# Optimization experiments

Hardware: AMD Instinct MI355X
Metric: run time of the kernel (lower is better)

The kernel has to match this reference:

```python
import jax, jax.numpy as jnp
from jax import lax
import numpy as np

B, H, W, C = 64, 224, 224, 3
OH, OW = 224, 224
EPS = 1e-3  # keras BatchNormalization default epsilon
FLAT = 52 * 52 * 10  # after conv7(valid)->pool2->conv5(valid)->pool2 on 224x224


def setup_inputs() -> dict:
    key = jax.random.key(0)
    ks = jax.random.split(key, 6)
    return {
        "x": jax.random.normal(ks[0], (B, H, W, C), jnp.float32),
        "c1_w": jax.random.normal(ks[1], (7, 7, C, 8), jnp.float32) * 0.05,
        "c1_b": jnp.zeros((8,), jnp.float32),
        "g1": jnp.ones((8,), jnp.float32),
        "b1": jnp.zeros((8,), jnp.float32),
        "m1": jnp.zeros((8,), jnp.float32),
        "v1": jnp.ones((8,), jnp.float32),
        "c2_w": jax.random.normal(ks[2], (5, 5, 8, 10), jnp.float32) * 0.05,
        "c2_b": jnp.zeros((10,), jnp.float32),
        "g2": jnp.ones((10,), jnp.float32),
        "b2": jnp.zeros((10,), jnp.float32),
        "m2": jnp.zeros((10,), jnp.float32),
        "v2": jnp.ones((10,), jnp.float32),
        "d1_w": jax.random.normal(ks[3], (FLAT, 32), jnp.float32) * 0.01,
        "d1_b": jnp.zeros((32,), jnp.float32),
        "d2_w": jax.random.normal(ks[4], (32, 6), jnp.float32) * 0.01,
        "d2_b": jnp.array([1.0, 0.0, 0.0, 0.0, 1.0, 0.0], jnp.float32),  # identity affine
    }


def _conv(x, w, b):
    return lax.conv_general_dilated(x, w, (1, 1), 'VALID',
                                    dimension_numbers=('NHWC', 'HWIO', 'NHWC')) + b


def _maxpool(x):
    return lax.reduce_window(x, -jnp.inf, lax.max, (1, 2, 2, 1), (1, 2, 2, 1), 'VALID')


def _bn(x, g, b, m, v):
    # inference-mode batchnorm: gamma*(x-mean)/sqrt(var+eps)+beta
    return (x - m) * lax.rsqrt(v + EPS) * g + b


def _bilinear(img, px, py):
    # img: [H,W,C]; px,py: [OH,OW] pixel-space sample coords; zero fill outside
    x0 = jnp.floor(px).astype(jnp.int32)
    y0 = jnp.floor(py).astype(jnp.int32)

    def gather(yi, xi):
        valid = (yi >= 0) & (yi < H) & (xi >= 0) & (xi < W)
        v = img[jnp.clip(yi, 0, H - 1), jnp.clip(xi, 0, W - 1)]  # [OH,OW,C]
        return v * valid[..., None]

    wx = (px - x0)[..., None]
    wy = (py - y0)[..., None]
    return (gather(y0, x0) * (1 - wx) * (1 - wy)
            + gather(y0, x0 + 1) * wx * (1 - wy)
            + gather(y0 + 1, x0) * (1 - wx) * wy
            + gather(y0 + 1, x0 + 1) * wx * wy)


def reference(x, c1_w, c1_b, g1, b1, m1, v1, c2_w, c2_b, g2, b2, m2, v2,
              d1_w, d1_b, d2_w, d2_b):
    # localization network
    h = _maxpool(_bn(jax.nn.relu(_conv(x, c1_w, c1_b)), g1, b1, m1, v1))
    h = _maxpool(_bn(jax.nn.relu(_conv(h, c2_w, c2_b)), g2, b2, m2, v2))
    h = h.reshape(h.shape[0], -1)                      # [B, FLAT]
    h = jax.nn.relu(h @ d1_w + d1_b)                   # [B, 32]
    theta = (h @ d2_w + d2_b).reshape(-1, 2, 3)        # [B, 2, 3]

    # normalized homogeneous grid [N,3] with N = OH*OW
    xs = jnp.linspace(-1.0, 1.0, OW)
    ys = jnp.linspace(-1.0, 1.0, OH)
    xg, yg = jnp.meshgrid(xs, ys)
    grid = jnp.stack([xg.ravel(), yg.ravel(), jnp.ones(OH * OW, jnp.float32)], axis=-1)

    coords = jnp.einsum('bij,nj->bni', theta, grid)    # [B, N, 2]
    px = ((coords[..., 0] + 1.0) * 0.5 * (W - 1)).reshape(-1, OH, OW)
    py = ((coords[..., 1] + 1.0) * 0.5 * (H - 1)).reshape(-1, OH, OW)
    return jax.vmap(_bilinear)(x, px, py)              # [B, OH, OW, C]
```

## Files before the change

kernel.cpp:

```cpp
#include <hip/hip_runtime.h>
#include <hip/hip_bf16.h>


#define NCHUNK 423
#define KC 64

__global__ __launch_bounds__(256, 8) void k_conv1(
    const float* __restrict__ x, const float* __restrict__ w,
    const float* __restrict__ bias, const float* __restrict__ g,
    const float* __restrict__ bt, const float* __restrict__ m,
    const float* __restrict__ v, float* __restrict__ out, int zbase) {
  __shared__ float s_in[3][38][42];
  __shared__ float s_bn[3][8];
  const int tid = threadIdx.x;
  const int bx = blockIdx.x, by = blockIdx.y, b = zbase + blockIdx.z;

  if (tid < 8) {
    float sc = g[tid] * rsqrtf(v[tid] + 1e-3f);
    s_bn[0][tid] = sc;
    s_bn[1][tid] = bt[tid] - m[tid] * sc;
    s_bn[2][tid] = bias[tid];
  }
  const int iy0 = by * 32, ix0 = bx * 32;
  const float* xb = x + (size_t)b * 224 * 224 * 3;
  for (int f = tid; f < 38 * 114; f += 256) {
    int r = f / 114, rem = f - r * 114;
    int q = rem / 3, c = rem - q * 3;
    int gy = iy0 + r; if (gy > 223) gy = 223;
    int gc = ix0 + q; if (gc > 223) gc = 223;
    s_in[c][r][q] = xb[(gy * 224 + gc) * 3 + c];
  }
  __syncthreads();

  const int pxl = tid & 15, pyl = tid >> 4;
  const int lx = 2 * pxl, ly = 2 * pyl;
  float acc[2][2][8];
#pragma unroll
  for (int pr = 0; pr < 2; ++pr)
#pragma unroll
    for (int pc = 0; pc < 2; ++pc)
#pragma unroll
      for (int co = 0; co < 8; ++co) acc[pr][pc][co] = 0.f;

#pragma unroll 1
  for (int ci = 0; ci < 3; ++ci) {
    float rw[8][8];
#pragma unroll
    for (int r = 0; r < 8; ++r)
#pragma unroll
      for (int j = 0; j < 4; ++j) {
        float2 t = *(const float2*)&s_in[ci][ly + r][lx + 2 * j];
        rw[r][2 * j] = t.x; rw[r][2 * j + 1] = t.y;
      }
#pragma unroll
    for (int ky = 0; ky < 7; ++ky) {
      float wv[7][8];
#pragma unroll
      for (int kx = 0; kx < 7; ++kx) {
        const float* wp = w + ((ky * 7 + kx) * 3 + ci) * 8;
        float4 a = *(const float4*)wp;
        float4 c4 = *(const float4*)(wp + 4);
        wv[kx][0] = a.x;  wv[kx][1] = a.y;  wv[kx][2] = a.z;  wv[kx][3] = a.w;
        wv[kx][4] = c4.x; wv[kx][5] = c4.y; wv[kx][6] = c4.z; wv[kx][7] = c4.w;
      }
#pragma unroll
      for (int kx = 0; kx < 7; ++kx)
#pragma unroll
        for (int pr = 0; pr < 2; ++pr)
#pragma unroll
          for (int pc = 0; pc < 2; ++pc) {
            float iv = rw[ky + pr][kx + pc];
#pragma unroll
            for (int co = 0; co < 8; ++co)
              acc[pr][pc][co] = fmaf(iv, wv[kx][co], acc[pr][pc][co]);
          }
    }
  }

  const int py = by * 16 + pyl, px = bx * 16 + pxl;
  if (py < 109 && px < 109) {
#pragma unroll
    for (int co = 0; co < 8; ++co) {
      float sc = s_bn[0][co], sh = s_bn[1][co], bs = s_bn[2][co];
      float a0 = fmaxf(acc[0][0][co] + bs, 0.f) * sc + sh;
      float a1 = fmaxf(acc[0][1][co] + bs, 0.f) * sc + sh;
      float a2 = fmaxf(acc[1][0][co] + bs, 0.f) * sc + sh;
      float a3 = fmaxf(acc[1][1][co] + bs, 0.f) * sc + sh;
      out[((size_t)co * 64 + b) * 109 * 110 + py * 110 + px] =
          fmaxf(fmaxf(a0, a1), fmaxf(a2, a3));
    }
  }
}

__global__ __launch_bounds__(256) void k_conv2(
    const float* __restrict__ in, const float* __restrict__ w,
    const float* __restrict__ bias, const float* __restrict__ g,
    const float* __restrict__ bt, const float* __restrict__ m,
    const float* __restrict__ v, float* __restrict__ out) {
  __shared__ float s_in[8][36][38];
  __shared__ float s_bn[3][10];
  const int tid = threadIdx.x;
  const int bx = blockIdx.x, by = blockIdx.y, b = blockIdx.z;

  if (tid < 10) {
    float sc = g[tid] * rsqrtf(v[tid] + 1e-3f);
    s_bn[0][tid] = sc;
    s_bn[1][tid] = bt[tid] - m[tid] * sc;
    s_bn[2][tid] = bias[tid];
  }
  const int iy0 = by * 32, ix0 = bx * 32;
  for (int f = tid; f < 8 * 36 * 36; f += 256) {
    int ci = f / 1296, rem = f - ci * 1296;
    int r = rem / 36, q = rem - r * 36;
    int gy = iy0 + r; if (gy > 108) gy = 108;
    int gc = ix0 + q; if (gc > 108) gc = 108;
    s_in[ci][r][q] = in[(((size_t)ci * 64 + b) * 109 + gy) * 110 + gc];
  }
  __syncthreads();

  const int pxl = tid & 15, pyl = tid >> 4;
  const int lx = 2 * pxl, ly = 2 * pyl;
  float acc[2][2][10];
#pragma unroll
  for (int pr = 0; pr < 2; ++pr)
#pragma unroll
    for (int pc = 0; pc < 2; ++pc)
#pragma unroll
      for (int co = 0; co < 10; ++co) acc[pr][pc][co] = 0.f;

#pragma unroll 1
  for (int ci = 0; ci < 8; ++ci) {
    float rw[6][8];
#pragma unroll
    for (int r = 0; r < 6; ++r)
#pragma unroll
      for (int j = 0; j < 4; ++j) {
        float2 t = *(const float2*)&s_in[ci][ly + r][lx + 2 * j];
        rw[r][2 * j] = t.x; rw[r][2 * j + 1] = t.y;
      }
#pragma unroll
    for (int ky = 0; ky < 5; ++ky) {
      float wv[5][10];
#pragma unroll
      for (int kx = 0; kx < 5; ++kx) {
        const float* wp = w + ((ky * 5 + kx) * 8 + ci) * 10;
#pragma unroll
        for (int u = 0; u < 5; ++u) {
          float2 t = *(const float2*)(wp + 2 * u);
          wv[kx][2 * u] = t.x; wv[kx][2 * u + 1] = t.y;
        }
      }
#pragma unroll
      for (int kx = 0; kx < 5; ++kx)
#pragma unroll
        for (int pr = 0; pr < 2; ++pr)
#pragma unroll
          for (int pc = 0; pc < 2; ++pc) {
            float iv = rw[ky + pr][kx + pc];
#pragma unroll
            for (int co = 0; co < 10; ++co)
              acc[pr][pc][co] = fmaf(iv, wv[kx][co], acc[pr][pc][co]);
          }
    }
  }

  const int py = by * 16 + pyl, px = bx * 16 + pxl;
  if (py < 52 && px < 52) {
    float res[10];
#pragma unroll
    for (int co = 0; co < 10; ++co) {
      float sc = s_bn[0][co], sh = s_bn[1][co], bs = s_bn[2][co];
      float a0 = fmaxf(acc[0][0][co] + bs, 0.f) * sc + sh;
      float a1 = fmaxf(acc[0][1][co] + bs, 0.f) * sc + sh;
      float a2 = fmaxf(acc[1][0][co] + bs, 0.f) * sc + sh;
      float a3 = fmaxf(acc[1][1][co] + bs, 0.f) * sc + sh;
      res[co] = fmaxf(fmaxf(a0, a1), fmaxf(a2, a3));
    }
    float2* op2 = (float2*)&out[(((size_t)b * 52 + py) * 52 + px) * 10];
#pragma unroll
    for (int i = 0; i < 5; i++)
      op2[i] = make_float2(res[2 * i], res[2 * i + 1]);
  }
}

__global__ __launch_bounds__(256) void k_fc1(
    const float* __restrict__ act, const float* __restrict__ w,
    float* __restrict__ partial) {
  __shared__ float s_a[64][KC];
  __shared__ float s_w[KC * 32];
  const int tid = threadIdx.x;
  const int chunk = blockIdx.x;
  const int k0 = chunk * KC;
  for (int f = tid; f < 64 * KC; f += 256) {
    int row = f >> 6, j = f & (KC - 1);
    int k = k0 + j;
    s_a[row][j] = (k < 27040) ? act[(size_t)row * 27040 + k] : 0.f;
  }
  for (int f = tid; f < KC * 32; f += 256) {
    int k = k0 + (f >> 5);
    s_w[f] = (k < 27040) ? w[(size_t)k0 * 32 + f] : 0.f;
  }
  __syncthreads();
  const int o = tid & 31, gg = tid >> 5;
  float sums[8];
#pragma unroll
  for (int i = 0; i < 8; i++) sums[i] = 0.f;
#pragma unroll 2
  for (int j = 0; j < KC; j += 4) {
    float w0 = s_w[j * 32 + o];
    float w1 = s_w[(j + 1) * 32 + o];
    float w2 = s_w[(j + 2) * 32 + o];
    float w3 = s_w[(j + 3) * 32 + o];
#pragma unroll
    for (int i = 0; i < 8; i++) {
      float4 av = *(const float4*)&s_a[gg * 8 + i][j];
      sums[i] = fmaf(av.x, w0, sums[i]);
      sums[i] = fmaf(av.y, w1, sums[i]);
      sums[i] = fmaf(av.z, w2, sums[i]);
      sums[i] = fmaf(av.w, w3, sums[i]);
    }
  }
#pragma unroll
  for (int i = 0; i < 8; i++)
    partial[((size_t)chunk * 64 + gg * 8 + i) * 32 + o] = sums[i];
}

__global__ __launch_bounds__(256) void k_fc2(
    const float* __restrict__ partial, const float* __restrict__ d1b,
    const float* __restrict__ d2w, const float* __restrict__ d2b,
    float* __restrict__ theta) {
  const int b = blockIdx.x;
  const int t = threadIdx.x;
  const int o = t & 31, seg = t >> 5;
  const int c0 = (seg < 7) ? seg * 53 : 371;
  const int cnt = (seg < 7) ? 53 : 52;
  float s = 0.f;
  for (int c = c0; c < c0 + cnt; ++c)
    s += partial[((size_t)c * 64 + b) * 32 + o];
  __shared__ float s_red[8][33];
  s_red[seg][o] = s;
  __syncthreads();
  __shared__ float s_h[32];
  if (t < 32) {
    float tot = 0.f;
#pragma unroll
    for (int sg = 0; sg < 8; ++sg) tot += s_red[sg][t];
    s_h[t] = fmaxf(tot + d1b[t], 0.f);
  }
  __syncthreads();
  if (t < 6) {
    float th = d2b[t];
#pragma unroll
    for (int o2 = 0; o2 < 32; o2++) th = fmaf(s_h[o2], d2w[o2 * 6 + t], th);
    theta[b * 6 + t] = th;
  }
}

__global__ __launch_bounds__(256) void k_sample(
    const float* __restrict__ x, const float* __restrict__ theta,
    float* __restrict__ out) {
  const int b = blockIdx.y;
  __shared__ float th[6];
  if (threadIdx.x < 6) th[threadIdx.x] = theta[b * 6 + threadIdx.x];
  __syncthreads();
  const int t = blockIdx.x * 256 + threadIdx.x;
  const int oy = t / 224, ox = t - oy * 224;
  const float xn = -1.f + (2.f / 223.f) * (float)ox;
  const float yn = -1.f + (2.f / 223.f) * (float)oy;
  const float cx = th[0] * xn + th[1] * yn + th[2];
  const float cy = th[3] * xn + th[4] * yn + th[5];
  const float px = (cx + 1.f) * 0.5f * 223.f;
  const float py = (cy + 1.f) * 0.5f * 223.f;
  const float x0f = floorf(px), y0f = floorf(py);
  const int x0 = (int)x0f, y0 = (int)y0f;
  const float wx = px - x0f, wy = py - y0f;
  const float* xb = x + (size_t)b * 224 * 224 * 3;
  float a0 = 0.f, a1 = 0.f, a2 = 0.f;
#pragma unroll
  for (int dy = 0; dy < 2; dy++) {
    const int yi = y0 + dy;
    const bool vy = (yi >= 0) && (yi < 224);
    const int yc = yi < 0 ? 0 : (yi > 223 ? 223 : yi);
    const float wyv = dy ? wy : 1.f - wy;
#pragma unroll
    for (int dx = 0; dx < 2; dx++) {
      const int xi = x0 + dx;
      const bool vx = (xi >= 0) && (xi < 224);
      const int xc = xi < 0 ? 0 : (xi > 223 ? 223 : xi);
      const float wv = wyv * (dx ? wx : 1.f - wx) * ((vx && vy) ? 1.f : 0.f);
      const float* p = &xb[(yc * 224 + xc) * 3];
      a0 = fmaf(p[0], wv, a0);
      a1 = fmaf(p[1], wv, a1);
      a2 = fmaf(p[2], wv, a2);
    }
  }
  float* op = &out[((size_t)b * 50176 + t) * 3];
  op[0] = a0; op[1] = a1; op[2] = a2;
}

extern "C" void kernel_launch(void* const* d_in, const int* in_sizes, int n_in,
                              void* d_out, int out_size, void* d_ws, size_t ws_size,
                              hipStream_t stream) {
  const float* x    = (const float*)d_in[0];
  const float* c1w  = (const float*)d_in[1];
  const float* c1b  = (const float*)d_in[2];
  const float* g1   = (const float*)d_in[3];
  const float* b1   = (const float*)d_in[4];
  const float* m1   = (const float*)d_in[5];
  const float* v1   = (const float*)d_in[6];
  const float* c2w  = (const float*)d_in[7];
  const float* c2b  = (const float*)d_in[8];
  const float* g2   = (const float*)d_in[9];
  const float* b2   = (const float*)d_in[10];
  const float* m2   = (const float*)d_in[11];
  const float* v2   = (const float*)d_in[12];
  const float* d1w  = (const float*)d_in[13];
  const float* d1b  = (const float*)d_in[14];
  const float* d2w  = (const float*)d_in[15];
  const float* d2b  = (const float*)d_in[16];
  float* out = (float*)d_out;

  float* ws = (float*)d_ws;
  float* p1    = ws;
  float* p2    = p1 + 6138880;
  float* theta = p2 + 1730560;
  float* part  = ws;

  for (int zb = 0; zb < 64; zb += 16)
    k_conv1<<<dim3(7, 7, 16), 256, 0, stream>>>(x, c1w, c1b, g1, b1, m1, v1, p1, zb);
  k_conv2<<<dim3(4, 4, 64), 256, 0, stream>>>(p1, c2w, c2b, g2, b2, m2, v2, p2);
  k_fc1<<<NCHUNK, 256, 0, stream>>>(p2, d1w, part);
  k_fc2<<<64, 256, 0, stream>>>(part, d1b, d2w, d2b, theta);
  k_sample<<<dim3(196, 64), 256, 0, stream>>>(x, theta, out);
}
```

Measured before the change: 328.3 us.

## Merge conv1 launches, retile conv2 by full-width row strips, vectorize sampler stores

conv1 now runs as a single launch over all 64 images instead of four launches, and its occupancy hint is dropped. conv2 is retiled into full-width 8-row strips that load the input channels in two halves of four. This removes the wasted halo and padding of the old 4x4 tile grid, but leaves 12 of every 64 threads idle. The sampler computes two output pixels per thread and writes them with float2 stores, which cuts launch overhead and issues wider writes.

```diff
diff --git a/kernel.cpp b/kernel.cpp
--- a/kernel.cpp
+++ b/kernel.cpp
@@ -5,15 +5,15 @@
 #define NCHUNK 423
 #define KC 64
 
-__global__ __launch_bounds__(256, 8) void k_conv1(
+__global__ __launch_bounds__(256) void k_conv1(
     const float* __restrict__ x, const float* __restrict__ w,
     const float* __restrict__ bias, const float* __restrict__ g,
     const float* __restrict__ bt, const float* __restrict__ m,
-    const float* __restrict__ v, float* __restrict__ out, int zbase) {
+    const float* __restrict__ v, float* __restrict__ out) {
   __shared__ float s_in[3][38][42];
   __shared__ float s_bn[3][8];
   const int tid = threadIdx.x;
-  const int bx = blockIdx.x, by = blockIdx.y, b = zbase + blockIdx.z;
+  const int bx = blockIdx.x, by = blockIdx.y, b = blockIdx.z;
 
   if (tid < 8) {
     float sc = g[tid] * rsqrtf(v[tid] + 1e-3f);
@@ -97,10 +97,10 @@
     const float* __restrict__ bias, const float* __restrict__ g,
     const float* __restrict__ bt, const float* __restrict__ m,
     const float* __restrict__ v, float* __restrict__ out) {
-  __shared__ float s_in[8][36][38];
+  __shared__ float s_in[4][12][110];
   __shared__ float s_bn[3][10];
   const int tid = threadIdx.x;
-  const int bx = blockIdx.x, by = blockIdx.y, b = blockIdx.z;
+  const int by = blockIdx.x, b = blockIdx.y;
 
   if (tid < 10) {
     float sc = g[tid] * rsqrtf(v[tid] + 1e-3f);
@@ -108,18 +108,10 @@
     s_bn[1][tid] = bt[tid] - m[tid] * sc;
     s_bn[2][tid] = bias[tid];
   }
-  const int iy0 = by * 32, ix0 = bx * 32;
-  for (int f = tid; f < 8 * 36 * 36; f += 256) {
-    int ci = f / 1296, rem = f - ci * 1296;
-    int r = rem / 36, q = rem - r * 36;
-    int gy = iy0 + r; if (gy > 108) gy = 108;
-    int gc = ix0 + q; if (gc > 108) gc = 108;
-    s_in[ci][r][q] = in[(((size_t)ci * 64 + b) * 109 + gy) * 110 + gc];
-  }
-  __syncthreads();
-
-  const int pxl = tid & 15, pyl = tid >> 4;
-  const int lx = 2 * pxl, ly = 2 * pyl;
+  const int iy0 = by * 8;
+  const int tx = tid & 63, ty = tid >> 6;
+  const int lx = 2 * tx, ly = 2 * ty;
+  const bool active = tx < 52;
   float acc[2][2][10];
 #pragma unroll
   for (int pr = 0; pr < 2; ++pr)
@@ -129,43 +121,56 @@
       for (int co = 0; co < 10; ++co) acc[pr][pc][co] = 0.f;
 
 #pragma unroll 1
-  for (int ci = 0; ci < 8; ++ci) {
-    float rw[6][8];
-#pragma unroll
-    for (int r = 0; r < 6; ++r)
-#pragma unroll
-      for (int j = 0; j < 4; ++j) {
-        float2 t = *(const float2*)&s_in[ci][ly + r][lx + 2 * j];
-        rw[r][2 * j] = t.x; rw[r][2 * j + 1] = t.y;
-      }
-#pragma unroll
-    for (int ky = 0; ky < 5; ++ky) {
-      float wv[5][10];
-#pragma unroll
-      for (int kx = 0; kx < 5; ++kx) {
-        const float* wp = w + ((ky * 5 + kx) * 8 + ci) * 10;
-#pragma unroll
-        for (int u = 0; u < 5; ++u) {
-          float2 t = *(const float2*)(wp + 2 * u);
-          wv[kx][2 * u] = t.x; wv[kx][2 * u + 1] = t.y;
+  for (int ph = 0; ph < 2; ++ph) {
+    if (ph) __syncthreads();
+    for (int f = tid; f < 4 * 12 * 108; f += 256) {
+      int c = f / 1296, rem = f - c * 1296;
+      int r = rem / 108, q = rem - r * 108;
+      s_in[c][r][q] = in[(((size_t)(ph * 4 + c) * 64 + b) * 109 + iy0 + r) * 110 + q];
+    }
+    __syncthreads();
+
+    if (active) {
+#pragma unroll 1
+      for (int c = 0; c < 4; ++c) {
+        float rw[6][8];
+#pragma unroll
+        for (int r = 0; r < 6; ++r)
+#pragma unroll
+          for (int j = 0; j < 4; ++j) {
+            float2 t = *(const float2*)&s_in[c][ly + r][lx + 2 * j];
+            rw[r][2 * j] = t.x; rw[r][2 * j + 1] = t.y;
+          }
+#pragma unroll
+        for (int ky = 0; ky < 5; ++ky) {
+          float wv[5][10];
+#pragma unroll
+          for (int kx = 0; kx < 5; ++kx) {
+            const float* wp = w + ((ky * 5 + kx) * 8 + ph * 4 + c) * 10;
+#pragma unroll
+            for (int u = 0; u < 5; ++u) {
+              float2 t = *(const float2*)(wp + 2 * u);
+              wv[kx][2 * u] = t.x; wv[kx][2 * u + 1] = t.y;
+            }
+          }
+#pragma unroll
+          for (int kx = 0; kx < 5; ++kx)
+#pragma unroll
+            for (int pr = 0; pr < 2; ++pr)
+#pragma unroll
+              for (int pc = 0; pc < 2; ++pc) {
+                float iv = rw[ky + pr][kx + pc];
+#pragma unroll
+                for (int co = 0; co < 10; ++co)
+                  acc[pr][pc][co] = fmaf(iv, wv[kx][co], acc[pr][pc][co]);
+              }
         }
       }
-#pragma unroll
-      for (int kx = 0; kx < 5; ++kx)
-#pragma unroll
-        for (int pr = 0; pr < 2; ++pr)
-#pragma unroll
-          for (int pc = 0; pc < 2; ++pc) {
-            float iv = rw[ky + pr][kx + pc];
-#pragma unroll
-            for (int co = 0; co < 10; ++co)
-              acc[pr][pc][co] = fmaf(iv, wv[kx][co], acc[pr][pc][co]);
-          }
-    }
-  }
-
-  const int py = by * 16 + pyl, px = bx * 16 + pxl;
-  if (py < 52 && px < 52) {
+    }
+  }
+
+  if (active) {
+    const int py = by * 4 + ty, px = tx;
     float res[10];
 #pragma unroll
     for (int co = 0; co < 10; ++co) {
@@ -263,39 +268,47 @@
   __shared__ float th[6];
   if (threadIdx.x < 6) th[threadIdx.x] = theta[b * 6 + threadIdx.x];
   __syncthreads();
-  const int t = blockIdx.x * 256 + threadIdx.x;
-  const int oy = t / 224, ox = t - oy * 224;
-  const float xn = -1.f + (2.f / 223.f) * (float)ox;
-  const float yn = -1.f + (2.f / 223.f) * (float)oy;
-  const float cx = th[0] * xn + th[1] * yn + th[2];
-  const float cy = th[3] * xn + th[4] * yn + th[5];
-  const float px = (cx + 1.f) * 0.5f * 223.f;
-  const float py = (cy + 1.f) * 0.5f * 223.f;
-  const float x0f = floorf(px), y0f = floorf(py);
-  const int x0 = (int)x0f, y0 = (int)y0f;
-  const float wx = px - x0f, wy = py - y0f;
+  const int t0 = (blockIdx.x * 256 + threadIdx.x) * 2;
   const float* xb = x + (size_t)b * 224 * 224 * 3;
-  float a0 = 0.f, a1 = 0.f, a2 = 0.f;
-#pragma unroll
-  for (int dy = 0; dy < 2; dy++) {
-    const int yi = y0 + dy;
-    const bool vy = (yi >= 0) && (yi < 224);
-    const int yc = yi < 0 ? 0 : (yi > 223 ? 223 : yi);
-    const float wyv = dy ? wy : 1.f - wy;
-#pragma unroll
-    for (int dx = 0; dx < 2; dx++) {
-      const int xi = x0 + dx;
-      const bool vx = (xi >= 0) && (xi < 224);
-      const int xc = xi < 0 ? 0 : (xi > 223 ? 223 : xi);
-      const float wv = wyv * (dx ? wx : 1.f - wx) * ((vx && vy) ? 1.f : 0.f);
-      const float* p = &xb[(yc * 224 + xc) * 3];
-      a0 = fmaf(p[0], wv, a0);
-      a1 = fmaf(p[1], wv, a1);
-      a2 = fmaf(p[2], wv, a2);
-    }
-  }
-  float* op = &out[((size_t)b * 50176 + t) * 3];
-  op[0] = a0; op[1] = a1; op[2] = a2;
+  float res[2][3];
+#pragma unroll
+  for (int i = 0; i < 2; ++i) {
+    const int t = t0 + i;
+    const int oy = t / 224, ox = t - oy * 224;
+    const float xn = -1.f + (2.f / 223.f) * (float)ox;
+    const float yn = -1.f + (2.f / 223.f) * (float)oy;
+    const float cx = th[0] * xn + th[1] * yn + th[2];
+    const float cy = th[3] * xn + th[4] * yn + th[5];
+    const float px = (cx + 1.f) * 0.5f * 223.f;
+    const float py = (cy + 1.f) * 0.5f * 223.f;
+    const float x0f = floorf(px), y0f = floorf(py);
+    const int x0 = (int)x0f, y0 = (int)y0f;
+    const float wx = px - x0f, wy = py - y0f;
+    float a0 = 0.f, a1 = 0.f, a2 = 0.f;
+#pragma unroll
+    for (int dy = 0; dy < 2; dy++) {
+      const int yi = y0 + dy;
+      const bool vy = (yi >= 0) && (yi < 224);
+      const int yc = yi < 0 ? 0 : (yi > 223 ? 223 : yi);
+      const float wyv = dy ? wy : 1.f - wy;
+#pragma unroll
+      for (int dx = 0; dx < 2; dx++) {
+        const int xi = x0 + dx;
+        const bool vx = (xi >= 0) && (xi < 224);
+        const int xc = xi < 0 ? 0 : (xi > 223 ? 223 : xi);
+        const float wv = wyv * (dx ? wx : 1.f - wx) * ((vx && vy) ? 1.f : 0.f);
+        const float* p = &xb[(yc * 224 + xc) * 3];
+        a0 = fmaf(p[0], wv, a0);
+        a1 = fmaf(p[1], wv, a1);
+        a2 = fmaf(p[2], wv, a2);
+      }
+    }
+    res[i][0] = a0; res[i][1] = a1; res[i][2] = a2;
+  }
+  float2* op = (float2*)&out[((size_t)b * 50176 + t0) * 3];
+  op[0] = make_float2(res[0][0], res[0][1]);
+  op[1] = make_float2(res[0][2], res[1][0]);
+  op[2] = make_float2(res[1][1], res[1][2]);
 }
 
 extern "C" void kernel_launch(void* const* d_in, const int* in_sizes, int n_in,
@@ -326,10 +339,9 @@
   float* theta = p2 + 1730560;
   float* part  = ws;
 
-  for (int zb = 0; zb < 64; zb += 16)
-    k_conv1<<<dim3(7, 7, 16), 256, 0, stream>>>(x, c1w, c1b, g1, b1, m1, v1, p1, zb);
-  k_conv2<<<dim3(4, 4, 64), 256, 0, stream>>>(p1, c2w, c2b, g2, b2, m2, v2, p2);
+  k_conv1<<<dim3(7, 7, 64), 256, 0, stream>>>(x, c1w, c1b, g1, b1, m1, v1, p1);
+  k_conv2<<<dim3(13, 64), 256, 0, stream>>>(p1, c2w, c2b, g2, b2, m2, v2, p2);
   k_fc1<<<NCHUNK, 256, 0, stream>>>(p2, d1w, part);
   k_fc2<<<64, 256, 0, stream>>>(part, d1b, d2w, d2b, theta);
-  k_sample<<<dim3(196, 64), 256, 0, stream>>>(x, theta, out);
-}
+  k_sample<<<dim3(98, 64), 256, 0, stream>>>(x, theta, out);
+}
```

Result: faster. 275.3 us (-16.2%).
